# Kernel tuning notes

Measured on AMD Instinct MI355X. Metric: run time of the kernel, lower is better.

The kernel has to match this reference:

```python
import jax, jax.numpy as jnp
import numpy as np

B, N, K = 1, 100000, 16
C_IN, C_ADD, C_MID = 64, 16, 16
IN_F, OUT_F = (C_IN + C_ADD) * C_MID, 256


def setup_inputs() -> dict:
    key = jax.random.key(0)
    ks = jax.random.split(key, 8)
    return {
        "input_features": jax.random.normal(ks[0], (B, N, C_IN), dtype=jnp.float32),
        "neighbor_inds": jax.random.randint(ks[1], (B, N, K), 0, N, dtype=jnp.int32),
        "inverse_neighbors": jax.random.randint(ks[2], (B, N * K), 0, N, dtype=jnp.int32),
        "inverse_k": jax.random.randint(ks[3], (B, N + 1), 0, K, dtype=jnp.int32),
        "inverse_idx": jax.random.randint(ks[4], (B, N * K), 0, N * K, dtype=jnp.int32),
        "weightnet": jax.random.normal(ks[5], (B, N, K, C_MID), dtype=jnp.float32),
        "additional_features": jax.random.normal(ks[6], (B, N, K, C_ADD), dtype=jnp.float32),
        "linear_weights": jax.random.normal(ks[7], (OUT_F, IN_F), dtype=jnp.float32) * 0.02,
        "linear_bias": jnp.zeros((OUT_F,), dtype=jnp.float32),
    }


def reference(input_features, neighbor_inds, inverse_neighbors, inverse_k,
              inverse_idx, weightnet, additional_features,
              linear_weights, linear_bias):
    # Gather neighbor features: [B, N, K, C_in]
    gathered = jax.vmap(lambda f, idx: f[idx])(input_features, neighbor_inds)
    # Concatenate extra per-neighbor features: [B, N, K, C_in + C_add]
    feat = jnp.concatenate([gathered, additional_features], axis=-1)
    # WeightNet-weighted reduction over neighbors: [B, N, C, C_mid]
    pconv = jnp.einsum("bnkc,bnkm->bncm", feat, weightnet)
    pconv = pconv.reshape(pconv.shape[0], pconv.shape[1], -1)  # [B, N, C*C_mid]
    # Fused linear projection
    return pconv @ linear_weights.T + linear_bias
```

## Files before the change

kernel.cpp:

```cpp
#include <hip/hip_runtime.h>

#define NPTS 100000
#define PB 64
#define NBLK ((NPTS + PB - 1) / PB)
#define INF 1280
#define PSTR 544

using short8 = __attribute__((ext_vector_type(8))) short;
using f32x4  = __attribute__((ext_vector_type(4))) float;

__device__ __forceinline__ unsigned short f2bf(float x) {
  unsigned u = __float_as_uint(x);
  return (unsigned short)((u + 0x7FFFu + ((u >> 16) & 1u)) >> 16);
}
__device__ __forceinline__ unsigned pack2(float a, float b) {
  return (unsigned)f2bf(a) | ((unsigned)f2bf(b) << 16);
}

__global__ void k_prep(const float* __restrict__ in_f, unsigned short* __restrict__ inbf) {
  int i = blockIdx.x * 256 + threadIdx.x;
  if (i < 1600000) {
    float4 v = ((const float4*)in_f)[i];
    ushort4 o;
    o.x = f2bf(v.x); o.y = f2bf(v.y); o.z = f2bf(v.z); o.w = f2bf(v.w);
    ((ushort4*)inbf)[i] = o;
  }
}

__global__ void k_wconv(const float* __restrict__ W, unsigned short* __restrict__ Wb) {
  int g = blockIdx.x * 256 + threadIdx.x;
  int j = g & 7;
  int col = (g >> 3) & 15;
  int ks = (g >> 7) & 31;
  int rest = g >> 12;
  int ct = rest % 5, nt = rest / 5;
  int kh = ks * 8 + j;
  int m = kh >> 4, ci = kh & 15;
  Wb[g] = f2bf(W[(nt * 16 + col) * INF + (ct * 16 + ci) * 16 + m]);
}

__global__ __launch_bounds__(512, 4) void k_fused(
    const unsigned short* __restrict__ inbf, const int* __restrict__ nbr,
    const float* __restrict__ wn_g, const float* __restrict__ add_f,
    const unsigned short* __restrict__ Wb, const float* __restrict__ bias,
    float* __restrict__ out)
{
  __shared__ __align__(16) unsigned char sF[PB * PSTR];
  __shared__ __align__(16) unsigned char sA[PB * 528];

  const int t = threadIdx.x;
  const int w = t >> 6, lane = t & 63;
  const int g16 = lane >> 4, c16 = lane & 15;
  const long p0 = (long)blockIdx.x * PB;

  int uidx[4], upp[4];
#pragma unroll
  for (int i = 0; i < 4; ++i) {
    int flat = i * 512 + t;
    long pp = p0 + (flat >> 5); if (pp >= NPTS) pp = NPTS - 1;
    upp[i] = (int)pp;
    uidx[i] = nbr[pp * 16 + ((flat >> 1) & 15)];
  }

  uint4 sr[4];
  auto gload = [&](int ct) {
#pragma unroll
    for (int i = 0; i < 4; ++i) {
      int uh = (i * 512 + t) & 1;
      sr[i] = *(const uint4*)(inbf + (long)uidx[i] * 64 + ct * 16 + uh * 8);
    }
  };
  auto fload = [&]() {
#pragma unroll
    for (int i = 0; i < 4; ++i) {
      int flat = i * 512 + t, uk = (flat >> 1) & 15, uh = flat & 1;
      const float* s = add_f + (long)upp[i] * 256 + uk * 16 + uh * 8;
      float4 a = *(const float4*)s, b = *(const float4*)(s + 4);
      sr[i] = make_uint4(pack2(a.x, a.y), pack2(a.z, a.w), pack2(b.x, b.y), pack2(b.z, b.w));
    }
  };
  auto swrite = [&]() {
#pragma unroll
    for (int i = 0; i < 4; ++i) {
      int flat = i * 512 + t, up = flat >> 5, uk = (flat >> 1) & 15, uh = flat & 1;
      unsigned char* base = sF + up * PSTR + uh * 256 + uk * 2;
      *(unsigned short*)(base +   0) = (unsigned short)(sr[i].x);
      *(unsigned short*)(base +  32) = (unsigned short)(sr[i].x >> 16);
      *(unsigned short*)(base +  64) = (unsigned short)(sr[i].y);
      *(unsigned short*)(base +  96) = (unsigned short)(sr[i].y >> 16);
      *(unsigned short*)(base + 128) = (unsigned short)(sr[i].z);
      *(unsigned short*)(base + 160) = (unsigned short)(sr[i].z >> 16);
      *(unsigned short*)(base + 192) = (unsigned short)(sr[i].w);
      *(unsigned short*)(base + 224) = (unsigned short)(sr[i].w >> 16);
    }
  };

  gload(0);
#pragma unroll
  for (int i = 0; i < 4; ++i) {
    int flat = i * 512 + t, up = flat >> 5, uk = (flat >> 1) & 15, uh = flat & 1;
    const float* s = wn_g + (long)upp[i] * 256 + uk * 16 + uh * 8;
    float4 a = *(const float4*)s, b = *(const float4*)(s + 4);
    unsigned char* base = sF + up * PSTR + uh * 256 + uk * 2;
    *(unsigned short*)(base +   0) = f2bf(a.x);
    *(unsigned short*)(base +  32) = f2bf(a.y);
    *(unsigned short*)(base +  64) = f2bf(a.z);
    *(unsigned short*)(base +  96) = f2bf(a.w);
    *(unsigned short*)(base + 128) = f2bf(b.x);
    *(unsigned short*)(base + 160) = f2bf(b.y);
    *(unsigned short*)(base + 192) = f2bf(b.z);
    *(unsigned short*)(base + 224) = f2bf(b.w);
  }
  __syncthreads();

  short8 bfr[8];
#pragma unroll
  for (int i = 0; i < 8; ++i) {
    bfr[i] = (short8){0, 0, 0, 0, 0, 0, 0, 0};
    if (g16 < 2)
      bfr[i] = *(const short8*)(sF + (w * 8 + i) * PSTR + c16 * 32 + g16 * 16);
  }
  __syncthreads();

  auto pconv = [&]() {
#pragma unroll
    for (int g = 0; g < 2; ++g) {
      short8 af[4];
#pragma unroll
      for (int i = 0; i < 4; ++i) {
        af[i] = (short8){0, 0, 0, 0, 0, 0, 0, 0};
        if (g16 < 2)
          af[i] = *(const short8*)(sF + (w * 8 + g * 4 + i) * PSTR + c16 * 32 + g16 * 16);
      }
#pragma unroll
      for (int i = 0; i < 4; ++i) {
        int p = w * 8 + g * 4 + i;
        f32x4 d = __builtin_amdgcn_mfma_f32_16x16x32_bf16(
            af[i], bfr[g * 4 + i], (f32x4){0.f, 0.f, 0.f, 0.f}, 0, 0, 0);
        *(uint2*)(sA + p * 528 + c16 * 32 + g16 * 8) =
            make_uint2(pack2(d[0], d[1]), pack2(d[2], d[3]));
      }
    }
  };

  f32x4 acc[4][2];
#pragma unroll
  for (int rr = 0; rr < 4; ++rr)
#pragma unroll
    for (int ntl = 0; ntl < 2; ++ntl) acc[rr][ntl] = (f32x4){0.f, 0.f, 0.f, 0.f};

  auto gemm = [&](int ct) {
#pragma unroll
    for (int kl = 0; kl < 8; ++kl) {
      short8 a[4];
#pragma unroll
      for (int rr = 0; rr < 4; ++rr)
        a[rr] = *(const short8*)(sA + (rr * 16 + c16) * 528 + kl * 64 + g16 * 16);
#pragma unroll
      for (int ntl = 0; ntl < 2; ++ntl) {
        int nt = w * 2 + ntl;
        short8 b = *(const short8*)(Wb + ((long)((nt * 5 + ct) * 32 + kl * 4 + g16) * 16 + c16) * 8);
#pragma unroll
        for (int rr = 0; rr < 4; ++rr)
          acc[rr][ntl] = __builtin_amdgcn_mfma_f32_16x16x32_bf16(a[rr], b, acc[rr][ntl], 0, 0, 0);
      }
    }
  };

  swrite();
  __syncthreads();
  pconv();
  __syncthreads();
  for (int ct = 0; ct < 5; ++ct) {
    if (ct < 3) gload(ct + 1);
    else if (ct == 3) fload();
    gemm(ct);
    if (ct < 4) {
      swrite();
      __syncthreads();
      pconv();
      __syncthreads();
    }
  }

#pragma unroll
  for (int ntl = 0; ntl < 2; ++ntl) {
    int n = (w * 2 + ntl) * 16 + c16;
    float bv = bias[n];
#pragma unroll
    for (int rr = 0; rr < 4; ++rr) {
      long prow = p0 + rr * 16 + g16 * 4;
#pragma unroll
      for (int r = 0; r < 4; ++r)
        if (prow + r < NPTS) out[(prow + r) * 256 + n] = acc[rr][ntl][r] + bv;
    }
  }
}

extern "C" void kernel_launch(void* const* d_in, const int* in_sizes, int n_in,
                              void* d_out, int out_size, void* d_ws, size_t ws_size,
                              hipStream_t stream) {
  const float* in_f  = (const float*)d_in[0];
  const int*   nbr   = (const int*)d_in[1];
  const float* wn    = (const float*)d_in[5];
  const float* add_f = (const float*)d_in[6];
  const float* W     = (const float*)d_in[7];
  const float* bias  = (const float*)d_in[8];
  float* out = (float*)d_out;

  unsigned short* inbf = (unsigned short*)d_ws;
  unsigned short* Wb   = (unsigned short*)((char*)d_ws + 13631488);

  k_prep<<<dim3(6250), dim3(256), 0, stream>>>(in_f, inbf);
  k_wconv<<<dim3(1280), dim3(256), 0, stream>>>(W, Wb);
  k_fused<<<dim3(NBLK), dim3(512), 0, stream>>>(inbf, nbr, wn, add_f, Wb, bias, out);
}
```

Measured before the change: 254.3 us.

## Swizzle shared-memory layout and repack gathers into wide LDS stores

Replaces the padded shared buffers with a 512-byte-row XOR-swizzled layout for both the feature tile and the pconv output. Each thread now owns four neighbors of one point and transposes them in registers with byte permutes, so LDS writes become 8-byte stores instead of many 2-byte scattered stores. Neighbor indices are loaded as one int4, and the epilogue is lightly reorganized. This aims to cut LDS store instruction count and bank conflicts, at the cost of extra permute ALU work and an added barrier in the prologue.

```diff
diff --git a/kernel.cpp b/kernel.cpp
--- a/kernel.cpp
+++ b/kernel.cpp
@@ -4,7 +4,6 @@
 #define PB 64
 #define NBLK ((NPTS + PB - 1) / PB)
 #define INF 1280
-#define PSTR 544
 
 using short8 = __attribute__((ext_vector_type(8))) short;
 using f32x4  = __attribute__((ext_vector_type(4))) float;
@@ -15,6 +14,9 @@
 }
 __device__ __forceinline__ unsigned pack2(float a, float b) {
   return (unsigned)f2bf(a) | ((unsigned)f2bf(b) << 16);
+}
+__device__ __forceinline__ unsigned char* swzp(unsigned char* base, int row, int inrow) {
+  return base + row * 512 + ((inrow & ~15) ^ ((row & 15) << 4)) + (inrow & 15);
 }
 
 __global__ void k_prep(const float* __restrict__ in_f, unsigned short* __restrict__ inbf) {
@@ -45,72 +47,65 @@
     const unsigned short* __restrict__ Wb, const float* __restrict__ bias,
     float* __restrict__ out)
 {
-  __shared__ __align__(16) unsigned char sF[PB * PSTR];
-  __shared__ __align__(16) unsigned char sA[PB * 528];
+  __shared__ __align__(16) unsigned char sF[PB * 512];
+  __shared__ __align__(16) unsigned char sA[PB * 512];
 
   const int t = threadIdx.x;
   const int w = t >> 6, lane = t & 63;
   const int g16 = lane >> 4, c16 = lane & 15;
   const long p0 = (long)blockIdx.x * PB;
 
-  int uidx[4], upp[4];
-#pragma unroll
-  for (int i = 0; i < 4; ++i) {
-    int flat = i * 512 + t;
-    long pp = p0 + (flat >> 5); if (pp >= NPTS) pp = NPTS - 1;
-    upp[i] = (int)pp;
-    uidx[i] = nbr[pp * 16 + ((flat >> 1) & 15)];
-  }
-
-  uint4 sr[4];
+  const int up = t >> 3, uh = (t >> 2) & 1, ukq = t & 3;
+  long upp = p0 + up; if (upp >= NPTS) upp = NPTS - 1;
+  const int4 uidx = *(const int4*)&nbr[upp * 16 + ukq * 4];
+
+  unsigned gg[4][4];
+  unsigned pk[8][2];
+
   auto gload = [&](int ct) {
 #pragma unroll
-    for (int i = 0; i < 4; ++i) {
-      int uh = (i * 512 + t) & 1;
-      sr[i] = *(const uint4*)(inbf + (long)uidx[i] * 64 + ct * 16 + uh * 8);
-    }
-  };
-  auto fload = [&]() {
-#pragma unroll
-    for (int i = 0; i < 4; ++i) {
-      int flat = i * 512 + t, uk = (flat >> 1) & 15, uh = flat & 1;
-      const float* s = add_f + (long)upp[i] * 256 + uk * 16 + uh * 8;
-      float4 a = *(const float4*)s, b = *(const float4*)(s + 4);
-      sr[i] = make_uint4(pack2(a.x, a.y), pack2(a.z, a.w), pack2(b.x, b.y), pack2(b.z, b.w));
+    for (int j = 0; j < 4; ++j) {
+      int idx = ((const int*)&uidx)[j];
+      *(uint4*)&gg[j][0] = *(const uint4*)(inbf + (long)idx * 64 + ct * 16 + uh * 8);
+    }
+  };
+  auto packg = [&]() {
+#pragma unroll
+    for (int x = 0; x < 8; ++x) {
+      int wi = x >> 1;
+      unsigned sel = (x & 1) ? 0x07060302u : 0x05040100u;
+      pk[x][0] = __builtin_amdgcn_perm(gg[1][wi], gg[0][wi], sel);
+      pk[x][1] = __builtin_amdgcn_perm(gg[3][wi], gg[2][wi], sel);
+    }
+  };
+  auto floadpack = [&](const float* __restrict__ src) {
+    float4 av[4], bv[4];
+#pragma unroll
+    for (int j = 0; j < 4; ++j) {
+      const float* s = src + (upp * 16 + ukq * 4 + j) * 16 + uh * 8;
+      av[j] = *(const float4*)s;
+      bv[j] = *(const float4*)(s + 4);
+    }
+#pragma unroll
+    for (int x = 0; x < 8; ++x) {
+      int e = x & 3;
+      float e0 = (x < 4) ? ((const float*)&av[0])[e] : ((const float*)&bv[0])[e];
+      float e1 = (x < 4) ? ((const float*)&av[1])[e] : ((const float*)&bv[1])[e];
+      float e2 = (x < 4) ? ((const float*)&av[2])[e] : ((const float*)&bv[2])[e];
+      float e3 = (x < 4) ? ((const float*)&av[3])[e] : ((const float*)&bv[3])[e];
+      pk[x][0] = pack2(e0, e1);
+      pk[x][1] = pack2(e2, e3);
     }
   };
   auto swrite = [&]() {
 #pragma unroll
-    for (int i = 0; i < 4; ++i) {
-      int flat = i * 512 + t, up = flat >> 5, uk = (flat >> 1) & 15, uh = flat & 1;
-      unsigned char* base = sF + up * PSTR + uh * 256 + uk * 2;
-      *(unsigned short*)(base +   0) = (unsigned short)(sr[i].x);
-      *(unsigned short*)(base +  32) = (unsigned short)(sr[i].x >> 16);
-      *(unsigned short*)(base +  64) = (unsigned short)(sr[i].y);
-      *(unsigned short*)(base +  96) = (unsigned short)(sr[i].y >> 16);
-      *(unsigned short*)(base + 128) = (unsigned short)(sr[i].z);
-      *(unsigned short*)(base + 160) = (unsigned short)(sr[i].z >> 16);
-      *(unsigned short*)(base + 192) = (unsigned short)(sr[i].w);
-      *(unsigned short*)(base + 224) = (unsigned short)(sr[i].w >> 16);
-    }
+    for (int x = 0; x < 8; ++x)
+      *(uint2*)swzp(sF, up, (uh * 8 + x) * 32 + ukq * 8) = make_uint2(pk[x][0], pk[x][1]);
   };
 
   gload(0);
-#pragma unroll
-  for (int i = 0; i < 4; ++i) {
-    int flat = i * 512 + t, up = flat >> 5, uk = (flat >> 1) & 15, uh = flat & 1;
-    const float* s = wn_g + (long)upp[i] * 256 + uk * 16 + uh * 8;
-    float4 a = *(const float4*)s, b = *(const float4*)(s + 4);
-    unsigned char* base = sF + up * PSTR + uh * 256 + uk * 2;
-    *(unsigned short*)(base +   0) = f2bf(a.x);
-    *(unsigned short*)(base +  32) = f2bf(a.y);
-    *(unsigned short*)(base +  64) = f2bf(a.z);
-    *(unsigned short*)(base +  96) = f2bf(a.w);
-    *(unsigned short*)(base + 128) = f2bf(b.x);
-    *(unsigned short*)(base + 160) = f2bf(b.y);
-    *(unsigned short*)(base + 192) = f2bf(b.z);
-    *(unsigned short*)(base + 224) = f2bf(b.w);
-  }
+  floadpack(wn_g);
+  swrite();
   __syncthreads();
 
   short8 bfr[8];
@@ -118,8 +113,10 @@
   for (int i = 0; i < 8; ++i) {
     bfr[i] = (short8){0, 0, 0, 0, 0, 0, 0, 0};
     if (g16 < 2)
-      bfr[i] = *(const short8*)(sF + (w * 8 + i) * PSTR + c16 * 32 + g16 * 16);
-  }
+      bfr[i] = *(const short8*)swzp(sF, w * 8 + i, c16 * 32 + g16 * 16);
+  }
+  __syncthreads();
+  packg(); swrite();
   __syncthreads();
 
   auto pconv = [&]() {
@@ -130,18 +127,21 @@
       for (int i = 0; i < 4; ++i) {
         af[i] = (short8){0, 0, 0, 0, 0, 0, 0, 0};
         if (g16 < 2)
-          af[i] = *(const short8*)(sF + (w * 8 + g * 4 + i) * PSTR + c16 * 32 + g16 * 16);
+          af[i] = *(const short8*)swzp(sF, w * 8 + g * 4 + i, c16 * 32 + g16 * 16);
       }
 #pragma unroll
       for (int i = 0; i < 4; ++i) {
         int p = w * 8 + g * 4 + i;
         f32x4 d = __builtin_amdgcn_mfma_f32_16x16x32_bf16(
             af[i], bfr[g * 4 + i], (f32x4){0.f, 0.f, 0.f, 0.f}, 0, 0, 0);
-        *(uint2*)(sA + p * 528 + c16 * 32 + g16 * 8) =
+        *(uint2*)swzp(sA, p, c16 * 32 + g16 * 8) =
             make_uint2(pack2(d[0], d[1]), pack2(d[2], d[3]));
       }
     }
   };
+
+  pconv();
+  __syncthreads();
 
   f32x4 acc[4][2];
 #pragma unroll
@@ -155,7 +155,7 @@
       short8 a[4];
 #pragma unroll
       for (int rr = 0; rr < 4; ++rr)
-        a[rr] = *(const short8*)(sA + (rr * 16 + c16) * 528 + kl * 64 + g16 * 16);
+        a[rr] = *(const short8*)swzp(sA, rr * 16 + c16, kl * 64 + g16 * 16);
 #pragma unroll
       for (int ntl = 0; ntl < 2; ++ntl) {
         int nt = w * 2 + ntl;
@@ -167,15 +167,12 @@
     }
   };
 
-  swrite();
-  __syncthreads();
-  pconv();
-  __syncthreads();
   for (int ct = 0; ct < 5; ++ct) {
     if (ct < 3) gload(ct + 1);
-    else if (ct == 3) fload();
+    else if (ct == 3) floadpack(add_f);
     gemm(ct);
     if (ct < 4) {
+      if (ct < 3) packg();
       swrite();
       __syncthreads();
       pconv();
@@ -183,16 +180,18 @@
     }
   }
 
-#pragma unroll
-  for (int ntl = 0; ntl < 2; ++ntl) {
-    int n = (w * 2 + ntl) * 16 + c16;
-    float bv = bias[n];
-#pragma unroll
-    for (int rr = 0; rr < 4; ++rr) {
-      long prow = p0 + rr * 16 + g16 * 4;
-#pragma unroll
-      for (int r = 0; r < 4; ++r)
-        if (prow + r < NPTS) out[(prow + r) * 256 + n] = acc[rr][ntl][r] + bv;
+  float bv0 = bias[(w * 2 + 0) * 16 + c16];
+  float bv1 = bias[(w * 2 + 1) * 16 + c16];
+#pragma unroll
+  for (int rr = 0; rr < 4; ++rr) {
+#pragma unroll
+    for (int r = 0; r < 4; ++r) {
+      long prow = p0 + rr * 16 + g16 * 4 + r;
+      if (prow < NPTS) {
+        float* o = out + prow * 256 + c16;
+        o[(w * 2 + 0) * 16] = acc[rr][0][r] + bv0;
+        o[(w * 2 + 1) * 16] = acc[rr][1][r] + bv1;
+      }
     }
   }
 }
```

New measurement: 425.1 us. +67.2%, slower.
